# Kernel optimization log

Measured on AMD Instinct MI355X. Metric: run time of the kernel, lower is better.

The kernel has to match this reference:

```python
import math
import jax, jax.numpy as jnp
import numpy as np

HEADS = 8
DIM_HEAD = 32
DIM = 128
EPS_LN = 1e-5
EPS_NORM = 1e-12


def setup_inputs() -> dict:
    key = jax.random.key(0)
    ks = jax.random.split(key, 4)
    inner = HEADS * DIM_HEAD  # 256
    x = jax.random.normal(ks[0], (1, DIM, 16, 64, 64), dtype=jnp.float32)
    g = jnp.ones((1, DIM, 1, 1, 1), dtype=jnp.float32)
    b = jnp.zeros((1, DIM, 1, 1, 1), dtype=jnp.float32)
    w_qkv = jax.random.normal(ks[1], (3 * inner, DIM), dtype=jnp.float32) * 0.05
    w_out = jax.random.normal(ks[2], (DIM, inner), dtype=jnp.float32) * 0.05
    b_out = jnp.zeros((DIM,), dtype=jnp.float32)
    return {"x": x, "g": g, "b": b, "w_qkv": w_qkv, "w_out": w_out, "b_out": b_out}


def _l2norm_ch(t):
    # F.normalize(t, dim=1): divide by max(||t||_2, eps) along channel axis
    n = jnp.sqrt(jnp.sum(t * t, axis=1, keepdims=True))
    return t / jnp.maximum(n, EPS_NORM)


def _gather_axis(t, idx, axis):
    # t: [bh, c, D, H, W]; idx: [bh, kk]; gather along spatial `axis`
    shape = list(t.shape)
    shape[axis] = idx.shape[1]
    ix = idx.reshape((idx.shape[0],) + (1,) * (axis - 1) + (idx.shape[1],) + (1,) * (4 - axis))
    ix = jnp.broadcast_to(ix, shape)
    return jnp.take_along_axis(t, ix, axis=axis)


def _dpsa_forward(x, g, b, w_qkv, w_out, b_out):
    bsz, c, D, H, W = x.shape
    kd = int(math.ceil(D ** 0.5))
    kh = int(math.ceil(H ** 0.5))
    kw = int(math.ceil(W ** 0.5))

    # ChanLayerNorm3d (biased variance over channel dim)
    mean = jnp.mean(x, axis=1, keepdims=True)
    var = jnp.var(x, axis=1, keepdims=True)
    xn = (x - mean) / jnp.sqrt(var + EPS_LN) * g + b

    # 1x1x1 conv to qkv (no bias)
    qkv = jnp.einsum('oc,bcdhw->bodhw', w_qkv, xn)
    inner = HEADS * DIM_HEAD
    q, k, v = qkv[:, :inner], qkv[:, inner:2 * inner], qkv[:, 2 * inner:]

    def fold(t):  # b (i c) d h w -> (b i) c d h w
        return t.reshape(bsz * HEADS, DIM_HEAD, D, H, W)
    q, k, v = fold(q), fold(k), fold(v)
    D0, H0, W0 = D, H, W

    q = _l2norm_ch(q)
    k = _l2norm_ch(k)
    q_abs = jnp.abs(q)

    # depth pruning
    if kd < D:
        q_probe = q_abs.sum(axis=(3, 4))                 # [bh, c, D]
        k_probe = jnp.abs(k).sum(axis=(3, 4))            # [bh, c, D]
        score = jnp.einsum('bcd,bcd->bd', q_probe, k_probe)
        _, idx = jax.lax.top_k(score, kd)
        k = _gather_axis(k, idx, 2)
        v = _gather_axis(v, idx, 2)
        D = kd
    # height pruning
    if kh < H:
        q_probe = q_abs.sum(axis=(2, 4))                 # [bh, c, H]
        k_probe = jnp.abs(k).sum(axis=(2, 4))            # [bh, c, H]
        score = jnp.einsum('bch,bch->bh', q_probe, k_probe)
        _, idx = jax.lax.top_k(score, kh)
        k = _gather_axis(k, idx, 3)
        v = _gather_axis(v, idx, 3)
        H = kh
    # width pruning
    if kw < W:
        q_probe = q_abs.sum(axis=(2, 3))                 # [bh, c, W]
        k_probe = jnp.abs(k).sum(axis=(2, 3))            # [bh, c, W]
        score = jnp.einsum('bcw,bcw->bw', q_probe, k_probe)
        _, idx = jax.lax.top_k(score, kw)
        k = _gather_axis(k, idx, 4)
        v = _gather_axis(v, idx, 4)
        W = kw

    def flat(t):  # b c d h w -> b (dhw) c
        return t.reshape(t.shape[0], t.shape[1], -1).transpose(0, 2, 1)
    qf, kf, vf = flat(q), flat(k), flat(v)

    sim = jnp.einsum('bic,bjc->bij', qf, kf)  # note: original applies no scale
    attn = jax.nn.softmax(sim, axis=-1)
    out_flat = jnp.einsum('bij,bjc->bic', attn, vf)  # [bh, N, c]

    # faithful to torch .view: raw row-major reinterpretation
    out = out_flat.reshape(bsz * HEADS, DIM_HEAD, D0, H0, W0)
    out = out.reshape(bsz, HEADS * DIM_HEAD, D0, H0, W0)
    return jnp.einsum('oc,bcdhw->bodhw', w_out, out) + b_out[None, :, None, None, None]


def reference(x, g, b, w_qkv, w_out, b_out):
    return _dpsa_forward(x, g, b, w_qkv, w_out, b_out)
```

## Files before the change

kernel.cpp:

```cpp
#include <hip/hip_runtime.h>
#include <math.h>

#define P_TOT 65536
#define CH    128
#define NHEAD 8
#define KD    4
#define KH    8
#define KW    8
#define NJ    256

typedef unsigned short u16;
typedef unsigned int   u32;
typedef __attribute__((ext_vector_type(8))) short frag8;
typedef __attribute__((ext_vector_type(4))) float f32x4;

__device__ inline u16 bf16r(float a) {
    u32 ua = __float_as_uint(a);
    return (u16)((ua + 0x7fff + ((ua >> 16) & 1)) >> 16);
}
__device__ inline float bf16f(u16 h) {
    return __uint_as_float(((u32)h) << 16);
}
__device__ inline u32 packhl(float v) {
    u16 hh = bf16r(v);
    u16 ll = bf16r(v - bf16f(hh));
    return (u32)hh | ((u32)ll << 16);
}

__global__ __launch_bounds__(256) void k_ln(const float* __restrict__ x,
                                            const float* __restrict__ g,
                                            const float* __restrict__ b,
                                            u32* __restrict__ xnT_pk) {
    __shared__ u32 buf[64 * 131];
    __shared__ float red[8 * 64];
    __shared__ float stat[2 * 64];
    float* xt = (float*)buf;
    int t  = threadIdx.x;
    int p0 = blockIdx.x * 64;
    #pragma unroll
    for (int r = 0; r < 8; ++r) {
        int id = t + 256 * r;
        int c = id >> 4, q4 = id & 15;
        *(float4*)(xt + c * 64 + q4 * 4) =
            *(const float4*)(x + (size_t)c * P_TOT + p0 + q4 * 4);
    }
    __syncthreads();
    int pp = t & 63, part = t >> 6;
    float sum = 0.f, ssq = 0.f;
    for (int ci = 0; ci < 32; ++ci) {
        float v = xt[(part * 32 + ci) * 64 + pp];
        sum += v; ssq += v * v;
    }
    red[part * 64 + pp] = sum;
    red[256 + part * 64 + pp] = ssq;
    __syncthreads();
    if (t < 64) {
        float s = red[t] + red[64 + t] + red[128 + t] + red[192 + t];
        float q = red[256 + t] + red[320 + t] + red[384 + t] + red[448 + t];
        float mean = s * (1.f / CH);
        float var  = q * (1.f / CH) - mean * mean;
        stat[t] = mean;
        stat[64 + t] = 1.f / sqrtf(var + 1e-5f);
    }
    __syncthreads();
    float mean = stat[pp], inv = stat[64 + pp];
    u32 pk[32];
    for (int ci = 0; ci < 32; ++ci) {
        int c = part * 32 + ci;
        float v  = xt[c * 64 + pp];
        float xn = (v - mean) * inv * g[c] + b[c];
        pk[ci] = packhl(xn);
    }
    __syncthreads();
    u32* tr = buf;
    for (int ci = 0; ci < 32; ++ci)
        tr[pp * 131 + part * 32 + ci] = pk[ci];
    __syncthreads();
    #pragma unroll
    for (int r = 0; r < 8; ++r) {
        int id = t + 256 * r;
        int pr = id >> 5, ch = id & 31;
        const u32* srcp = tr + pr * 131 + ch * 4;
        uint4 v4;
        v4.x = srcp[0]; v4.y = srcp[1]; v4.z = srcp[2]; v4.w = srcp[3];
        *(uint4*)(xnT_pk + (size_t)(p0 + pr) * 128 + ch * 4) = v4;
    }
}

__global__ __launch_bounds__(256) void k_wsplit(const float* __restrict__ wqkv,
                                                const float* __restrict__ wout,
                                                u16* __restrict__ w_hi,
                                                u16* __restrict__ w_lo,
                                                u16* __restrict__ w2_hi,
                                                u16* __restrict__ w2_lo) {
    int id = blockIdx.x * 256 + threadIdx.x;
    if (id < 65536) {
        float v = wqkv[id];
        u16 hh = bf16r(v);
        w_hi[id] = hh; w_lo[id] = bf16r(v - bf16f(hh));
    } else {
        int j = id - 65536;
        float v = wout[j];
        u16 hh = bf16r(v);
        w2_hi[j] = hh; w2_lo[j] = bf16r(v - bf16f(hh));
    }
}

__global__ __launch_bounds__(256) void k_gemm_qkv(const u32* __restrict__ xnT_pk,
                                                  const u16* __restrict__ w_hi,
                                                  const u16* __restrict__ w_lo,
                                                  float* __restrict__ qk,
                                                  u16* __restrict__ qT) {
    __shared__ u16 a_hi[128 * 64], a_lo[128 * 64];
    __shared__ u16 b_hi[128 * 64], b_lo[128 * 64];
    int t    = threadIdx.x;
    int lane = t & 63, wave = t >> 6;
    int wp = wave & 1, wo = wave >> 1;
    int m = lane & 15, quad = lane >> 4;
    int p0 = blockIdx.x * 128;
    int o0 = blockIdx.y * 128;
    f32x4 acc[4][4] = {};
    for (int k0 = 0; k0 < 128; k0 += 64) {
        __syncthreads();
        #pragma unroll
        for (int r = 0; r < 4; ++r) {
            int id  = t + 256 * r;
            int row = id >> 3, gg = id & 7;
            int go  = (gg ^ (row & 7)) * 8;
            const u32* src = xnT_pk + (size_t)(p0 + row) * 128 + k0 + gg * 8;
            u32 pkk[8];
            *(uint4*)pkk       = *(const uint4*)src;
            *(uint4*)(pkk + 4) = *(const uint4*)(src + 4);
            u32 hi4[4], lo4[4];
            #pragma unroll
            for (int e = 0; e < 4; ++e) {
                hi4[e] = __builtin_amdgcn_perm(pkk[2*e+1], pkk[2*e], 0x05040100);
                lo4[e] = __builtin_amdgcn_perm(pkk[2*e+1], pkk[2*e], 0x07060302);
            }
            *(uint4*)(a_hi + row * 64 + go) = *(uint4*)hi4;
            *(uint4*)(a_lo + row * 64 + go) = *(uint4*)lo4;
            *(uint4*)(b_hi + row * 64 + go) =
                *(const uint4*)(w_hi + (size_t)(o0 + row) * 128 + k0 + gg * 8);
            *(uint4*)(b_lo + row * 64 + go) =
                *(const uint4*)(w_lo + (size_t)(o0 + row) * 128 + k0 + gg * 8);
        }
        __syncthreads();
        #pragma unroll
        for (int ks = 0; ks < 2; ++ks) {
            frag8 ah[4], al[4], bh[4], bl[4];
            #pragma unroll
            for (int i = 0; i < 4; ++i) {
                int row = wp * 64 + i * 16 + m;
                int gg  = (ks * 4 + quad) ^ (row & 7);
                ah[i] = *(const frag8*)(a_hi + row * 64 + gg * 8);
                al[i] = *(const frag8*)(a_lo + row * 64 + gg * 8);
            }
            #pragma unroll
            for (int j = 0; j < 4; ++j) {
                int row = wo * 64 + j * 16 + m;
                int gg  = (ks * 4 + quad) ^ (row & 7);
                bh[j] = *(const frag8*)(b_hi + row * 64 + gg * 8);
                bl[j] = *(const frag8*)(b_lo + row * 64 + gg * 8);
            }
            #pragma unroll
            for (int i = 0; i < 4; ++i)
                #pragma unroll
                for (int j = 0; j < 4; ++j) {
                    acc[i][j] = __builtin_amdgcn_mfma_f32_16x16x32_bf16(ah[i], bh[j], acc[i][j], 0, 0, 0);
                    acc[i][j] = __builtin_amdgcn_mfma_f32_16x16x32_bf16(ah[i], bl[j], acc[i][j], 0, 0, 0);
                    acc[i][j] = __builtin_amdgcn_mfma_f32_16x16x32_bf16(al[i], bh[j], acc[i][j], 0, 0, 0);
                }
        }
    }
    #pragma unroll
    for (int i = 0; i < 4; ++i) {
        #pragma unroll
        for (int jg = 0; jg < 2; ++jg) {
            f32x4 s;
            #pragma unroll
            for (int r = 0; r < 4; ++r)
                s[r] = acc[i][2 * jg][r] * acc[i][2 * jg][r]
                     + acc[i][2 * jg + 1][r] * acc[i][2 * jg + 1][r];
            #pragma unroll
            for (int mask = 1; mask <= 8; mask <<= 1) {
                s[0] += __shfl_xor(s[0], mask, 64);
                s[1] += __shfl_xor(s[1], mask, 64);
                s[2] += __shfl_xor(s[2], mask, 64);
                s[3] += __shfl_xor(s[3], mask, 64);
            }
            #pragma unroll
            for (int r = 0; r < 4; ++r) {
                float inv = 1.f / fmaxf(sqrtf(s[r]), 1e-12f);
                acc[i][2 * jg][r]     *= inv;
                acc[i][2 * jg + 1][r] *= inv;
            }
        }
    }
    #pragma unroll
    for (int i = 0; i < 4; ++i) {
        int p = p0 + wp * 64 + i * 16 + quad * 4;
        #pragma unroll
        for (int j = 0; j < 4; ++j) {
            int o = o0 + wo * 64 + j * 16 + m;
            float4 v;
            v.x = acc[i][j][0]; v.y = acc[i][j][1];
            v.z = acc[i][j][2]; v.w = acc[i][j][3];
            *(float4*)(qk + (size_t)o * P_TOT + p) = v;
        }
    }
    if (o0 < 256) {
        #pragma unroll
        for (int i = 0; i < 4; ++i) {
            #pragma unroll
            for (int j = 0; j < 4; ++j) {
                int grp = (o0 >> 5) + wo * 2 + (j >> 1);
                int cc  = (j & 1) * 16 + m;
                #pragma unroll
                for (int r = 0; r < 4; ++r) {
                    int p = p0 + wp * 64 + i * 16 + quad * 4 + r;
                    qT[((size_t)grp * P_TOT + p) * 32 + cc] = bf16r(acc[i][j][r]);
                }
            }
        }
    }
}

__global__ __launch_bounds__(256) void k_probe(const float* __restrict__ qk,
                                               float* __restrict__ pd,
                                               float* __restrict__ pdh,
                                               float* __restrict__ pdw) {
    int o = blockIdx.x;
    int d = blockIdx.y;
    int t = threadIdx.x;
    __shared__ float ph2[64 * 65];
    __shared__ float pwl[256];
    for (int i = t; i < 64 * 65; i += 256) ph2[i] = 0.f;
    __syncthreads();
    const float* src = qk + o * P_TOT + d * 4096;
    int col = t & 63;
    int tg  = t >> 6;
    float wsum = 0.f;
    #pragma unroll
    for (int r = 0; r < 16; ++r) {
        int i = t + 256 * r;
        float val = fabsf(src[i]);
        wsum += val;
        int h = 4 * r + tg;
        ph2[h * 65 + col] += val;
    }
    pwl[t] = wsum;
    __syncthreads();
    if (t < 64) {
        float s = 0.f;
        for (int cc = 0; cc < 64; ++cc) s += ph2[t * 65 + cc];
        pdh[(o * 16 + d) * 64 + t] = s;
        ph2[t * 65 + 64] = s;
    } else if (t < 128) {
        int w = t - 64;
        float s = 0.f;
        for (int g2 = 0; g2 < 4; ++g2) s += pwl[g2 * 64 + w];
        pdw[(o * 16 + d) * 64 + w] = s;
    }
    __syncthreads();
    if (t == 0) {
        float s = 0.f;
        for (int h = 0; h < 64; ++h) s += ph2[h * 65 + 64];
        pd[o * 16 + d] = s;
    }
}

__global__ __launch_bounds__(64) void k_psum(const float* __restrict__ pdh,
                                             const float* __restrict__ pdw,
                                             float* __restrict__ qph,
                                             float* __restrict__ qpw) {
    int o = blockIdx.x, t = threadIdx.x;
    float sh = 0.f, sw = 0.f;
    #pragma unroll
    for (int d = 0; d < 16; ++d) {
        sh += pdh[(o * 16 + d) * 64 + t];
        sw += pdw[(o * 16 + d) * 64 + t];
    }
    qph[o * 64 + t] = sh;
    qpw[o * 64 + t] = sw;
}

__global__ __launch_bounds__(64) void k_topk_d(const float* __restrict__ pd,
                                               int* __restrict__ idx_d) {
    int h = blockIdx.x, t = threadIdx.x;
    __shared__ float sc[16];
    if (t < 16) {
        float s = 0.f;
        for (int c = 0; c < 32; ++c)
            s += pd[(h * 32 + c) * 16 + t] * pd[(256 + h * 32 + c) * 16 + t];
        sc[t] = s;
    }
    __syncthreads();
    if (t == 0) {
        bool used[16] = {};
        for (int r = 0; r < KD; ++r) {
            int best = 0; float bv = -1e30f;
            for (int i = 0; i < 16; ++i)
                if (!used[i] && sc[i] > bv) { bv = sc[i]; best = i; }
            used[best] = true;
            idx_d[h * KD + r] = best;
        }
    }
}

__global__ __launch_bounds__(256) void k_topk_h(const float* __restrict__ qph,
                                                const float* __restrict__ pdh,
                                                const int* __restrict__ idx_d,
                                                int* __restrict__ idx_h) {
    int h = blockIdx.x, t = threadIdx.x;
    int tq = t & 63, cg = t >> 6;
    __shared__ float sc2[4][64];
    __shared__ float sc[64];
    int ds[KD];
    #pragma unroll
    for (int i = 0; i < KD; ++i) ds[i] = idx_d[h * KD + i];
    float partial = 0.f;
    for (int ci = 0; ci < 8; ++ci) {
        int c  = cg * 8 + ci;
        int oq = h * 32 + c, ok = 256 + h * 32 + c;
        float qp = qph[oq * 64 + tq];
        float kp = 0.f;
        #pragma unroll
        for (int i = 0; i < KD; ++i) kp += pdh[(ok * 16 + ds[i]) * 64 + tq];
        partial += qp * kp;
    }
    sc2[cg][tq] = partial;
    __syncthreads();
    if (t < 64) sc[t] = sc2[0][t] + sc2[1][t] + sc2[2][t] + sc2[3][t];
    __syncthreads();
    if (t == 0) {
        bool used[64] = {};
        for (int r = 0; r < KH; ++r) {
            int best = 0; float bv = -1e30f;
            for (int i = 0; i < 64; ++i)
                if (!used[i] && sc[i] > bv) { bv = sc[i]; best = i; }
            used[best] = true;
            idx_h[h * KH + r] = best;
        }
    }
}

__global__ __launch_bounds__(64) void k_probe_w(const float* __restrict__ qk,
                                                const int* __restrict__ idx_d,
                                                const int* __restrict__ idx_h,
                                                float* __restrict__ kpw) {
    int o2 = blockIdx.x;
    int w  = threadIdx.x;
    int h  = o2 >> 5;
    const float* src = qk + (256 + o2) * P_TOT;
    float s = 0.f;
    for (int i = 0; i < KD; ++i) {
        int pb = idx_d[h * KD + i] * 4096;
        for (int j = 0; j < KH; ++j)
            s += fabsf(src[pb + idx_h[h * KH + j] * 64 + w]);
    }
    kpw[o2 * 64 + w] = s;
}

__global__ __launch_bounds__(256) void k_topk_w(const float* __restrict__ qpw,
                                                const float* __restrict__ kpw,
                                                int* __restrict__ idx_w) {
    int h = blockIdx.x, t = threadIdx.x;
    int tq = t & 63, cg = t >> 6;
    __shared__ float sc2[4][64];
    __shared__ float sc[64];
    float partial = 0.f;
    for (int ci = 0; ci < 8; ++ci) {
        int c  = cg * 8 + ci;
        int oq = h * 32 + c;
        partial += qpw[oq * 64 + tq] * kpw[(h * 32 + c) * 64 + tq];
    }
    sc2[cg][tq] = partial;
    __syncthreads();
    if (t < 64) sc[t] = sc2[0][t] + sc2[1][t] + sc2[2][t] + sc2[3][t];
    __syncthreads();
    if (t == 0) {
        bool used[64] = {};
        for (int r = 0; r < KW; ++r) {
            int best = 0; float bv = -1e30f;
            for (int i = 0; i < 64; ++i)
                if (!used[i] && sc[i] > bv) { bv = sc[i]; best = i; }
            used[best] = true;
            idx_w[h * KW + r] = best;
        }
    }
}

__global__ __launch_bounds__(64) void k_gather(const float* __restrict__ qk,
                                               const u32* __restrict__ xnT_pk,
                                               const float* __restrict__ wqkv,
                                               const int* __restrict__ idx_d,
                                               const int* __restrict__ idx_h,
                                               const int* __restrict__ idx_w,
                                               u16* __restrict__ kb,
                                               u16* __restrict__ vT) {
    int h  = blockIdx.x;
    int jb = blockIdx.y;
    int t  = threadIdx.x;
    int j  = jb * 2 + (t >> 5);
    int c  = t & 31;
    int di = j >> 6, hi = (j >> 3) & 7, wi = j & 7;
    int p  = idx_d[h * KD + di] * 4096 + idx_h[h * KH + hi] * 64 + idx_w[h * KW + wi];
    kb[(h * NJ + j) * 32 + c] = bf16r(qk[(256 + h * 32 + c) * P_TOT + p]);
    const float* wr = wqkv + (512 + h * 32 + c) * CH;
    const u32* xp = xnT_pk + (size_t)p * 128;
    float acc = 0.f;
    for (int cc = 0; cc < CH; ++cc) {
        u32 pk = xp[cc];
        float v = __uint_as_float(pk << 16) + __uint_as_float(pk & 0xffff0000u);
        acc += wr[cc] * v;
    }
    int pos = (j & 0xE0) | ((j & 0x0C) << 1) | ((j & 0x10) >> 2) | (j & 3);
    vT[((size_t)h * 32 + c) * NJ + pos] = bf16r(acc);
}

__device__ inline frag8 mk_frag(uint2 a, uint2 b) {
    union { u32 u[4]; frag8 f; } v;
    v.u[0] = a.x; v.u[1] = a.y; v.u[2] = b.x; v.u[3] = b.y;
    return v.f;
}

__global__ __launch_bounds__(256) void k_attn(const u16* __restrict__ qT,
                                              const u16* __restrict__ kb,
                                              const u16* __restrict__ vT,
                                              u32* __restrict__ attn_pk) {
    __shared__ u16 sK[256 * 32];
    __shared__ u16 sV[32 * 264];
    int h    = blockIdx.x >> 8;
    int pc   = blockIdx.x & 255;
    int wave = threadIdx.x >> 6;
    int lane = threadIdx.x & 63;
    int m    = lane & 15;
    int quad = lane >> 4;
    int t    = threadIdx.x;

    int qbase = pc * 256 + wave * 64;
    frag8 bq[4];
    #pragma unroll
    for (int i = 0; i < 4; ++i)
        bq[i] = *(const frag8*)(qT + ((size_t)h * P_TOT + qbase + i * 16 + m) * 32 + quad * 8);

    const uint4* kg  = (const uint4*)(kb + (size_t)h * NJ * 32);
    uint4*       sKg = (uint4*)sK;
    #pragma unroll
    for (int r = 0; r < 4; ++r)
        sKg[t + 256 * r] = kg[t + 256 * r];
    const uint4* vg = (const uint4*)(vT + (size_t)h * 32 * NJ);
    #pragma unroll
    for (int r = 0; r < 4; ++r) {
        int g2 = t + 256 * r;
        int row = g2 >> 5, col = g2 & 31;
        *(uint4*)(sV + row * 264 + col * 8) = vg[g2];
    }
    __syncthreads();

    f32x4 zero = {0.f, 0.f, 0.f, 0.f};
    #pragma unroll
    for (int tile = 0; tile < 4; ++tile) {
        int p = qbase + tile * 16 + m;
        float den = 0.f;
        uint2 pk[16];
        #pragma unroll
        for (int tt = 0; tt < 16; ++tt) {
            frag8 ak = *(const frag8*)(sK + (tt * 16 + m) * 32 + quad * 8);
            f32x4 st = __builtin_amdgcn_mfma_f32_16x16x32_bf16(ak, bq[tile], zero, 0, 0, 0);
            float e0 = __expf(st[0]);
            float e1 = __expf(st[1]);
            float e2 = __expf(st[2]);
            float e3 = __expf(st[3]);
            den += (e0 + e1) + (e2 + e3);
            pk[tt].x = __builtin_amdgcn_perm(__float_as_uint(e1), __float_as_uint(e0), 0x07060302);
            pk[tt].y = __builtin_amdgcn_perm(__float_as_uint(e3), __float_as_uint(e2), 0x07060302);
        }
        den += __shfl_xor(den, 16, 64);
        den += __shfl_xor(den, 32, 64);

        f32x4 a0e = zero, a0o = zero, a1e = zero, a1o = zero;
        #pragma unroll
        for (int jc = 0; jc < 8; jc += 2) {
            frag8 bp0  = mk_frag(pk[2 * jc],     pk[2 * jc + 1]);
            frag8 bp1  = mk_frag(pk[2 * jc + 2], pk[2 * jc + 3]);
            frag8 av00 = *(const frag8*)(sV + m * 264 + jc * 32 + quad * 8);
            frag8 av01 = *(const frag8*)(sV + m * 264 + (jc + 1) * 32 + quad * 8);
            frag8 av10 = *(const frag8*)(sV + (16 + m) * 264 + jc * 32 + quad * 8);
            frag8 av11 = *(const frag8*)(sV + (16 + m) * 264 + (jc + 1) * 32 + quad * 8);
            a0e = __builtin_amdgcn_mfma_f32_16x16x32_bf16(av00, bp0, a0e, 0, 0, 0);
            a0o = __builtin_amdgcn_mfma_f32_16x16x32_bf16(av01, bp1, a0o, 0, 0, 0);
            a1e = __builtin_amdgcn_mfma_f32_16x16x32_bf16(av10, bp0, a1e, 0, 0, 0);
            a1o = __builtin_amdgcn_mfma_f32_16x16x32_bf16(av11, bp1, a1o, 0, 0, 0);
        }
        f32x4 acc0 = a0e + a0o;
        f32x4 acc1 = a1e + a1o;
        float inv = 1.f / den;
        size_t base = ((size_t)(h * 32 + (p >> 11))) * P_TOT + (size_t)(p & 2047) * 32;
        uint4 o0, o1;
        o0.x = packhl(acc0[0] * inv); o0.y = packhl(acc0[1] * inv);
        o0.z = packhl(acc0[2] * inv); o0.w = packhl(acc0[3] * inv);
        o1.x = packhl(acc1[0] * inv); o1.y = packhl(acc1[1] * inv);
        o1.z = packhl(acc1[2] * inv); o1.w = packhl(acc1[3] * inv);
        *(uint4*)(attn_pk + base + quad * 4)      = o0;
        *(uint4*)(attn_pk + base + 16 + quad * 4) = o1;
    }
}

__global__ __launch_bounds__(256) void k_gemm_out(const u32* __restrict__ attn_pk,
                                                  const u16* __restrict__ w2_hi,
                                                  const u16* __restrict__ w2_lo,
                                                  const float* __restrict__ bout,
                                                  float* __restrict__ out) {
    __shared__ u16 a_hi[128 * 64], a_lo[128 * 64];
    __shared__ u16 b_hi[128 * 64], b_lo[128 * 64];
    int t    = threadIdx.x;
    int lane = t & 63, wave = t >> 6;
    int wq = wave & 1, wo = wave >> 1;
    int m = lane & 15, quad = lane >> 4;
    int q0 = blockIdx.x * 128;
    f32x4 acc[4][4] = {};
    for (int k0 = 0; k0 < 256; k0 += 64) {
        __syncthreads();
        #pragma unroll
        for (int r = 0; r < 4; ++r) {
            int id = t + 256 * r;
            int qq = id & 127, gsel = id >> 7;
            u32 pkk[8];
            #pragma unroll
            for (int e = 0; e < 8; ++e)
                pkk[e] = attn_pk[(size_t)(k0 + gsel * 8 + e) * P_TOT + q0 + qq];
            u32 hi4[4], lo4[4];
            #pragma unroll
            for (int e = 0; e < 4; ++e) {
                hi4[e] = __builtin_amdgcn_perm(pkk[2*e+1], pkk[2*e], 0x05040100);
                lo4[e] = __builtin_amdgcn_perm(pkk[2*e+1], pkk[2*e], 0x07060302);
            }
            int go = (gsel ^ (qq & 7)) * 8;
            *(uint4*)(a_hi + qq * 64 + go) = *(uint4*)hi4;
            *(uint4*)(a_lo + qq * 64 + go) = *(uint4*)lo4;
        }
        #pragma unroll
        for (int r = 0; r < 4; ++r) {
            int id  = t + 256 * r;
            int row = id >> 3, gg = id & 7;
            int go  = (gg ^ (row & 7)) * 8;
            *(uint4*)(b_hi + row * 64 + go) =
                *(const uint4*)(w2_hi + (size_t)row * 256 + k0 + gg * 8);
            *(uint4*)(b_lo + row * 64 + go) =
                *(const uint4*)(w2_lo + (size_t)row * 256 + k0 + gg * 8);
        }
        __syncthreads();
        #pragma unroll
        for (int ks = 0; ks < 2; ++ks) {
            frag8 ah[4], al[4], bh[4], bl[4];
            #pragma unroll
            for (int i = 0; i < 4; ++i) {
                int row = wq * 64 + i * 16 + m;
                int gg  = (ks * 4 + quad) ^ (row & 7);
                ah[i] = *(const frag8*)(a_hi + row * 64 + gg * 8);
                al[i] = *(const frag8*)(a_lo + row * 64 + gg * 8);
            }
            #pragma unroll
            for (int j = 0; j < 4; ++j) {
                int row = wo * 64 + j * 16 + m;
                int gg  = (ks * 4 + quad) ^ (row & 7);
                bh[j] = *(const frag8*)(b_hi + row * 64 + gg * 8);
                bl[j] = *(const frag8*)(b_lo + row * 64 + gg * 8);
            }
            #pragma unroll
            for (int i = 0; i < 4; ++i)
                #pragma unroll
                for (int j = 0; j < 4; ++j) {
                    acc[i][j] = __builtin_amdgcn_mfma_f32_16x16x32_bf16(ah[i], bh[j], acc[i][j], 0, 0, 0);
                    acc[i][j] = __builtin_amdgcn_mfma_f32_16x16x32_bf16(ah[i], bl[j], acc[i][j], 0, 0, 0);
                    acc[i][j] = __builtin_amdgcn_mfma_f32_16x16x32_bf16(al[i], bh[j], acc[i][j], 0, 0, 0);
                }
        }
    }
    #pragma unroll
    for (int j = 0; j < 4; ++j) {
        int o = wo * 64 + j * 16 + m;
        float bv = bout[o];
        #pragma unroll
        for (int i = 0; i < 4; ++i) {
            int q = q0 + wq * 64 + i * 16 + quad * 4;
            float4 v;
            v.x = acc[i][j][0] + bv; v.y = acc[i][j][1] + bv;
            v.z = acc[i][j][2] + bv; v.w = acc[i][j][3] + bv;
            *(float4*)(out + (size_t)o * P_TOT + q) = v;
        }
    }
}

extern "C" void kernel_launch(void* const* d_in, const int* in_sizes, int n_in,
                              void* d_out, int out_size, void* d_ws, size_t ws_size,
                              hipStream_t stream) {
    const float* x    = (const float*)d_in[0];
    const float* g    = (const float*)d_in[1];
    const float* b    = (const float*)d_in[2];
    const float* wqkv = (const float*)d_in[3];
    const float* wout = (const float*)d_in[4];
    const float* bout = (const float*)d_in[5];
    float* out = (float*)d_out;
    float* ws  = (float*)d_ws;

    u32*   xnT_pk = (u32*)ws;
    float* qk   = ws + 8388608;
    u32*   attn_pk = (u32*)(qk + 256 * P_TOT);
    float* aux  = ws + 41943040;
    float* pd    = aux;
    float* pdh   = pd + 8192;
    float* pdw   = pdh + 524288;
    float* kpw   = pdw + 524288;
    float* qph   = kpw + 16384;
    float* qpw   = qph + 32768;
    int*   idx_d = (int*)(qpw + 32768);
    int*   idx_h = idx_d + 32;
    int*   idx_w = idx_h + 64;
    u16*   kb    = (u16*)(idx_w + 64);
    u16*   vT    = kb + 8 * NJ * 32;
    u16*   qT    = vT + 8 * 32 * NJ;
    u16*   w_hi  = qT + (size_t)8 * P_TOT * 32;
    u16*   w_lo  = w_hi + 512 * 128;
    u16*   w2_hi = w_lo + 512 * 128;
    u16*   w2_lo = w2_hi + 128 * 256;

    k_ln<<<1024, 256, 0, stream>>>(x, g, b, xnT_pk);
    k_wsplit<<<384, 256, 0, stream>>>(wqkv, wout, w_hi, w_lo, w2_hi, w2_lo);
    k_gemm_qkv<<<dim3(512, 4), 256, 0, stream>>>(xnT_pk, w_hi, w_lo, qk, qT);
    k_probe<<<dim3(512, 16), 256, 0, stream>>>(qk, pd, pdh, pdw);
    k_psum<<<512, 64, 0, stream>>>(pdh, pdw, qph, qpw);
    k_topk_d<<<8, 64, 0, stream>>>(pd, idx_d);
    k_topk_h<<<8, 256, 0, stream>>>(qph, pdh, idx_d, idx_h);
    k_probe_w<<<256, 64, 0, stream>>>(qk, idx_d, idx_h, kpw);
    k_topk_w<<<8, 256, 0, stream>>>(qpw, kpw, idx_w);
    k_gather<<<dim3(8, 128), 64, 0, stream>>>(qk, xnT_pk, wqkv,
                                              idx_d, idx_h, idx_w, kb, vT);
    k_attn<<<2048, 256, 0, stream>>>(qT, kb, vT, attn_pk);
    k_gemm_out<<<512, 256, 0, stream>>>(attn_pk, w2_hi, w2_lo, bout, out);
}
```

Baseline: 346.9 us.

## Store LN output as separate hi/lo bf16 planes and stage qT writes through LDS

The layer-norm kernel now writes two separate bf16 planes (hi and lo) instead of interleaved packed u32, so the QKV GEMM loads its A tiles directly with 16-byte copies and no per-element permute. The swizzle moves from the LDS store address to the global load address. The qT epilogue now stages bf16 results in shared memory and writes coalesced uint4 rows, replacing scattered 2-byte global stores. The cost is extra barriers and LDS reuse in the GEMM epilogue, plus two separate loads per element in the gather kernel.

After: 341.2 us. No clear change (-1.6%).

```diff
diff --git a/kernel.cpp b/kernel.cpp
--- a/kernel.cpp
+++ b/kernel.cpp
@@ -30,7 +30,8 @@
 __global__ __launch_bounds__(256) void k_ln(const float* __restrict__ x,
                                             const float* __restrict__ g,
                                             const float* __restrict__ b,
-                                            u32* __restrict__ xnT_pk) {
+                                            u16* __restrict__ xn_hi,
+                                            u16* __restrict__ xn_lo) {
     __shared__ u32 buf[64 * 131];
     __shared__ float red[8 * 64];
     __shared__ float stat[2 * 64];
@@ -81,9 +82,15 @@
         int id = t + 256 * r;
         int pr = id >> 5, ch = id & 31;
         const u32* srcp = tr + pr * 131 + ch * 4;
-        uint4 v4;
-        v4.x = srcp[0]; v4.y = srcp[1]; v4.z = srcp[2]; v4.w = srcp[3];
-        *(uint4*)(xnT_pk + (size_t)(p0 + pr) * 128 + ch * 4) = v4;
+        u32 v0 = srcp[0], v1 = srcp[1], v2 = srcp[2], v3 = srcp[3];
+        uint2 hv, lv;
+        hv.x = __builtin_amdgcn_perm(v1, v0, 0x05040100);
+        hv.y = __builtin_amdgcn_perm(v3, v2, 0x05040100);
+        lv.x = __builtin_amdgcn_perm(v1, v0, 0x07060302);
+        lv.y = __builtin_amdgcn_perm(v3, v2, 0x07060302);
+        size_t off = (size_t)(p0 + pr) * 128 + ch * 4;
+        *(uint2*)(xn_hi + off) = hv;
+        *(uint2*)(xn_lo + off) = lv;
     }
 }
 
@@ -106,13 +113,17 @@
     }
 }
 
-__global__ __launch_bounds__(256) void k_gemm_qkv(const u32* __restrict__ xnT_pk,
+__global__ __launch_bounds__(256) void k_gemm_qkv(const u16* __restrict__ xn_hi,
+                                                  const u16* __restrict__ xn_lo,
                                                   const u16* __restrict__ w_hi,
                                                   const u16* __restrict__ w_lo,
                                                   float* __restrict__ qk,
                                                   u16* __restrict__ qT) {
-    __shared__ u16 a_hi[128 * 64], a_lo[128 * 64];
-    __shared__ u16 b_hi[128 * 64], b_lo[128 * 64];
+    __shared__ u16 smem[4 * 128 * 64];
+    u16* a_hi = smem;
+    u16* a_lo = smem + 8192;
+    u16* b_hi = smem + 16384;
+    u16* b_lo = smem + 24576;
     int t    = threadIdx.x;
     int lane = t & 63, wave = t >> 6;
     int wp = wave & 1, wo = wave >> 1;
@@ -126,23 +137,14 @@
         for (int r = 0; r < 4; ++r) {
             int id  = t + 256 * r;
             int row = id >> 3, gg = id & 7;
-            int go  = (gg ^ (row & 7)) * 8;
-            const u32* src = xnT_pk + (size_t)(p0 + row) * 128 + k0 + gg * 8;
-            u32 pkk[8];
-            *(uint4*)pkk       = *(const uint4*)src;
-            *(uint4*)(pkk + 4) = *(const uint4*)(src + 4);
-            u32 hi4[4], lo4[4];
-            #pragma unroll
-            for (int e = 0; e < 4; ++e) {
-                hi4[e] = __builtin_amdgcn_perm(pkk[2*e+1], pkk[2*e], 0x05040100);
-                lo4[e] = __builtin_amdgcn_perm(pkk[2*e+1], pkk[2*e], 0x07060302);
-            }
-            *(uint4*)(a_hi + row * 64 + go) = *(uint4*)hi4;
-            *(uint4*)(a_lo + row * 64 + go) = *(uint4*)lo4;
-            *(uint4*)(b_hi + row * 64 + go) =
-                *(const uint4*)(w_hi + (size_t)(o0 + row) * 128 + k0 + gg * 8);
-            *(uint4*)(b_lo + row * 64 + go) =
-                *(const uint4*)(w_lo + (size_t)(o0 + row) * 128 + k0 + gg * 8);
+            int gs  = gg ^ (row & 7);
+            int dst = row * 64 + gg * 8;
+            size_t sa = (size_t)(p0 + row) * 128 + k0 + gs * 8;
+            size_t sb = (size_t)(o0 + row) * 128 + k0 + gs * 8;
+            *(uint4*)(a_hi + dst) = *(const uint4*)(xn_hi + sa);
+            *(uint4*)(a_lo + dst) = *(const uint4*)(xn_lo + sa);
+            *(uint4*)(b_hi + dst) = *(const uint4*)(w_hi + sb);
+            *(uint4*)(b_lo + dst) = *(const uint4*)(w_lo + sb);
         }
         __syncthreads();
         #pragma unroll
@@ -209,18 +211,29 @@
         }
     }
     if (o0 < 256) {
-        #pragma unroll
-        for (int i = 0; i < 4; ++i) {
+        __syncthreads();
+        u16* qtb = smem;
+        #pragma unroll
+        for (int i = 0; i < 4; ++i)
             #pragma unroll
             for (int j = 0; j < 4; ++j) {
-                int grp = (o0 >> 5) + wo * 2 + (j >> 1);
-                int cc  = (j & 1) * 16 + m;
+                int grp = wo * 2 + (j >> 1);
+                int c   = (j & 1) * 16 + m;
                 #pragma unroll
                 for (int r = 0; r < 4; ++r) {
-                    int p = p0 + wp * 64 + i * 16 + quad * 4 + r;
-                    qT[((size_t)grp * P_TOT + p) * 32 + cc] = bf16r(acc[i][j][r]);
+                    int pl = wp * 64 + i * 16 + quad * 4 + r;
+                    qtb[grp * 5120 + pl * 40 + c] = bf16r(acc[i][j][r]);
                 }
             }
+        __syncthreads();
+        int gbase = o0 >> 5;
+        #pragma unroll
+        for (int ri = 0; ri < 8; ++ri) {
+            int id = t + 256 * ri;
+            int grp = id >> 9, rem = id & 511;
+            int pl = rem >> 2, cq = rem & 3;
+            uint4 v = *(const uint4*)(qtb + grp * 5120 + pl * 40 + cq * 8);
+            *(uint4*)(qT + ((size_t)(gbase + grp) * P_TOT + p0 + pl) * 32 + cq * 8) = v;
         }
     }
 }
@@ -391,7 +404,8 @@
 }
 
 __global__ __launch_bounds__(64) void k_gather(const float* __restrict__ qk,
-                                               const u32* __restrict__ xnT_pk,
+                                               const u16* __restrict__ xn_hi,
+                                               const u16* __restrict__ xn_lo,
                                                const float* __restrict__ wqkv,
                                                const int* __restrict__ idx_d,
                                                const int* __restrict__ idx_h,
@@ -407,11 +421,11 @@
     int p  = idx_d[h * KD + di] * 4096 + idx_h[h * KH + hi] * 64 + idx_w[h * KW + wi];
     kb[(h * NJ + j) * 32 + c] = bf16r(qk[(256 + h * 32 + c) * P_TOT + p]);
     const float* wr = wqkv + (512 + h * 32 + c) * CH;
-    const u32* xp = xnT_pk + (size_t)p * 128;
+    const u16* xh = xn_hi + (size_t)p * 128;
+    const u16* xl = xn_lo + (size_t)p * 128;
     float acc = 0.f;
     for (int cc = 0; cc < CH; ++cc) {
-        u32 pk = xp[cc];
-        float v = __uint_as_float(pk << 16) + __uint_as_float(pk & 0xffff0000u);
+        float v = bf16f(xh[cc]) + bf16f(xl[cc]);
         acc += wr[cc] * v;
     }
     int pos = (j & 0xE0) | ((j & 0x0C) << 1) | ((j & 0x10) >> 2) | (j & 3);
@@ -605,7 +619,8 @@
     float* out = (float*)d_out;
     float* ws  = (float*)d_ws;
 
-    u32*   xnT_pk = (u32*)ws;
+    u16*   xn_hi = (u16*)ws;
+    u16*   xn_lo = xn_hi + (size_t)128 * P_TOT;
     float* qk   = ws + 8388608;
     u32*   attn_pk = (u32*)(qk + 256 * P_TOT);
     float* aux  = ws + 41943040;
@@ -626,16 +641,16 @@
     u16*   w2_hi = w_lo + 512 * 128;
     u16*   w2_lo = w2_hi + 128 * 256;
 
-    k_ln<<<1024, 256, 0, stream>>>(x, g, b, xnT_pk);
+    k_ln<<<1024, 256, 0, stream>>>(x, g, b, xn_hi, xn_lo);
     k_wsplit<<<384, 256, 0, stream>>>(wqkv, wout, w_hi, w_lo, w2_hi, w2_lo);
-    k_gemm_qkv<<<dim3(512, 4), 256, 0, stream>>>(xnT_pk, w_hi, w_lo, qk, qT);
+    k_gemm_qkv<<<dim3(512, 4), 256, 0, stream>>>(xn_hi, xn_lo, w_hi, w_lo, qk, qT);
     k_probe<<<dim3(512, 16), 256, 0, stream>>>(qk, pd, pdh, pdw);
     k_psum<<<512, 64, 0, stream>>>(pdh, pdw, qph, qpw);
     k_topk_d<<<8, 64, 0, stream>>>(pd, idx_d);
     k_topk_h<<<8, 256, 0, stream>>>(qph, pdh, idx_d, idx_h);
     k_probe_w<<<256, 64, 0, stream>>>(qk, idx_d, idx_h, kpw);
     k_topk_w<<<8, 256, 0, stream>>>(qpw, kpw, idx_w);
-    k_gather<<<dim3(8, 128), 64, 0, stream>>>(qk, xnT_pk, wqkv,
+    k_gather<<<dim3(8, 128), 64, 0, stream>>>(qk, xn_hi, xn_lo, wqkv,
                                               idx_d, idx_h, idx_w, kb, vT);
     k_attn<<<2048, 256, 0, stream>>>(qT, kb, vT, attn_pk);
     k_gemm_out<<<512, 256, 0, stream>>>(attn_pk, w2_hi, w2_lo, bout, out);
```
